# Performance work log

Measured on AMD Instinct MI355X. Metric: run time of the kernel, lower is better.

## Reference

```python
import jax, jax.numpy as jnp
import numpy as np
import math

H = 8
D_MODEL = 4096
D_K = D_MODEL // H  # 512; Sk must equal D_K for the im_attn @ value matmul
B, SQ, SK = 4, 2048, 512


def _linear_params(key, fan_in, fan_out):
    kw, kb = jax.random.split(key)
    bound = 1.0 / math.sqrt(fan_in)
    W = jax.random.uniform(kw, (fan_out, fan_in), jnp.float32, -bound, bound)
    b = jax.random.uniform(kb, (fan_out,), jnp.float32, -bound, bound)
    return W, b


def setup_inputs() -> dict:
    key = jax.random.key(0)
    ks = jax.random.split(key, 8)
    query = jax.random.normal(ks[0], (B, SQ, D_MODEL), jnp.float32)
    k_in = jax.random.normal(ks[1], (B, SK, D_MODEL), jnp.float32)
    v_in = jax.random.normal(ks[2], (B, SK, D_MODEL), jnp.float32)
    image_feat = jax.random.normal(ks[3], (B, SK, D_MODEL), jnp.float32)
    W0, b0 = _linear_params(ks[4], D_MODEL, D_MODEL)
    W1, b1 = _linear_params(ks[5], D_MODEL, D_MODEL)
    W2, b2 = _linear_params(ks[6], D_MODEL, D_MODEL)
    W3, b3 = _linear_params(ks[7], D_MODEL, D_MODEL)  # reused for image_feat AND output proj (as in source)
    return {"query": query, "key": k_in, "value": v_in, "image_feat": image_feat,
            "W0": W0, "b0": b0, "W1": W1, "b1": b1, "W2": W2, "b2": b2, "W3": W3, "b3": b3}


def _split_heads(x):
    # [b, s, d_model] -> [b, h, s, d_k]
    b, s, _ = x.shape
    return x.reshape(b, s, H, D_K).transpose(0, 2, 1, 3)


def reference(query, key, value, image_feat, W0, b0, W1, b1, W2, b2, W3, b3):
    q = _split_heads(query @ W0.T + b0)        # [b,h,Sq,d_k]
    k = _split_heads(key @ W1.T + b1)          # [b,h,Sk,d_k]
    v = _split_heads(value @ W2.T + b2)        # [b,h,Sk,d_k]
    imf = _split_heads(image_feat @ W3.T + b3) # [b,h,Sk,d_k]

    scores = jnp.einsum('bhqd,bhkd->bhqk', q, k) / math.sqrt(D_K)  # [b,h,Sq,Sk]
    p_attn = jax.nn.softmax(scores, axis=-1)
    # second-stage attention over feature axis (Sk == d_k so shapes line up)
    im_attn = jax.nn.softmax(jnp.einsum('bhqk,bhkd->bhqd', p_attn, imf), axis=-1)  # [b,h,Sq,d_k]
    x = jnp.einsum('bhqs,bhsd->bhqd', im_attn, v)  # contracts d_k axis of im_attn with Sk axis of v

    x = x.transpose(0, 2, 1, 3).reshape(query.shape[0], -1, H * D_K)  # [b,Sq,d_model]
    return x @ W3.T + b3  # linears[-1] is the same (shared) 4th linear
```

## Files before the change

### kernel.cpp

```cpp
#include <hip/hip_runtime.h>
#include <hip/hip_bf16.h>
#include <stdint.h>

#define B_   4
#define H_   8
#define SQ_  2048
#define SK_  512
#define DM_  4096
#define DK_  512

typedef __bf16 bf16;
typedef __bf16 bf16x8 __attribute__((ext_vector_type(8)));
typedef float  fx4    __attribute__((ext_vector_type(4)));

typedef __attribute__((address_space(1))) void gv_t;
typedef __attribute__((address_space(3))) void lv_t;

__global__ void sniff_dtype(const uint32_t* __restrict__ q, int* __restrict__ flag)
{
    const int l = threadIdx.x;
    int cnt = 0;
    #pragma unroll
    for (int i = 0; i < 4; ++i) {
        const uint32_t u = q[l * 4 + i];
        const int e = (u >> 7) & 0xFF;
        cnt += (e >= 100 && e <= 135) ? 1 : 0;
    }
    #pragma unroll
    for (int s = 1; s < 64; s <<= 1) cnt += __shfl_xor(cnt, s);
    if (l == 0) *flag = (cnt < 150) ? 1 : 0;
}

__global__ __launch_bounds__(256) void cvt_to_bf16(
    const void* __restrict__ in, bf16* __restrict__ out, const int* __restrict__ flagp)
{
    const size_t i = ((size_t)blockIdx.x * 256 + threadIdx.x) * 8;
    if (*flagp) {
        const float4* p = (const float4*)((const float*)in + i);
        const float4 u0 = p[0], u1 = p[1];
        bf16x8 v;
        v[0] = (bf16)u0.x; v[1] = (bf16)u0.y; v[2] = (bf16)u0.z; v[3] = (bf16)u0.w;
        v[4] = (bf16)u1.x; v[5] = (bf16)u1.y; v[6] = (bf16)u1.z; v[7] = (bf16)u1.w;
        *(bf16x8*)(out + i) = v;
    } else {
        *(bf16x8*)(out + i) = *(const bf16x8*)((const bf16*)in + i);
    }
}

__global__ __launch_bounds__(256, 3) void gemm_bt(
    const bf16* __restrict__ A, const bf16* __restrict__ Bt,
    void* __restrict__ Cv, const void* __restrict__ biasv,
    int K, int lda, int ldb, int ldc, float alpha,
    long long sAb, long long sAh, long long sBb, long long sBh,
    long long sCb, long long sCh,
    const int* __restrict__ flagp, int ebits)
{
    __shared__ bf16 sA[128 * 64];
    __shared__ bf16 sB[128 * 64];

    const int fl = ebits ? *flagp : 0;
    const bool bias32 = fl && (ebits & 1);
    const bool c32    = fl && (ebits & 2);

    const int z = blockIdx.z;
    const int bz = z >> 3, hz = z & 7;
    const bf16* Ab = A  + (size_t)bz * sAb + (size_t)hz * sAh;
    const bf16* Bb = Bt + (size_t)bz * sBb + (size_t)hz * sBh;
    const size_t offC = (size_t)bz * sCb + (size_t)hz * sCh;

    const int n0 = blockIdx.x * 128;
    const int m0 = blockIdx.y * 128;

    const int t = threadIdx.x;
    const int w = t >> 6, l = t & 63;
    const int lrow = l >> 3, lcol = l & 7;
    const int wm = (w >> 1) * 64, wn = (w & 1) * 64;
    const int ml = l & 15, quad = l >> 4;

    const bf16* pa[4];
    const bf16* pb[4];
    #pragma unroll
    for (int i = 0; i < 4; ++i) {
        const int c = w * 4 + i;
        const int r = c * 8 + lrow;
        const int jj = lcol ^ (r & 7);
        pa[i] = Ab + (size_t)(m0 + r) * lda + jj * 8;
        pb[i] = Bb + (size_t)(n0 + r) * ldb + jj * 8;
    }

    fx4 acc[4][4];
    const fx4 zero = {0.f, 0.f, 0.f, 0.f};
    #pragma unroll
    for (int i = 0; i < 4; ++i)
        #pragma unroll
        for (int j = 0; j < 4; ++j) acc[i][j] = zero;

    for (int kt = 0; kt < K; kt += 64) {
        #pragma unroll
        for (int i = 0; i < 4; ++i) {
            const int c = w * 4 + i;
            __builtin_amdgcn_global_load_lds((gv_t*)(pa[i] + kt), (lv_t*)(sA + c * 512), 16, 0, 0);
            __builtin_amdgcn_global_load_lds((gv_t*)(pb[i] + kt), (lv_t*)(sB + c * 512), 16, 0, 0);
        }
        __syncthreads();

        #pragma unroll
        for (int kk = 0; kk < 64; kk += 32) {
            bf16x8 af[4], bfr[4];
            const int jbase = (kk >> 3) + quad;
            #pragma unroll
            for (int mi = 0; mi < 4; ++mi) {
                const int r = wm + mi * 16 + ml;
                af[mi] = *(const bf16x8*)&sA[r * 64 + ((jbase ^ (r & 7)) << 3)];
            }
            #pragma unroll
            for (int ni = 0; ni < 4; ++ni) {
                const int r = wn + ni * 16 + ml;
                bfr[ni] = *(const bf16x8*)&sB[r * 64 + ((jbase ^ (r & 7)) << 3)];
            }
            #pragma unroll
            for (int mi = 0; mi < 4; ++mi)
                #pragma unroll
                for (int ni = 0; ni < 4; ++ni)
                    acc[mi][ni] = __builtin_amdgcn_mfma_f32_16x16x32_bf16(
                        af[mi], bfr[ni], acc[mi][ni], 0, 0, 0);
        }
        __syncthreads();
    }

    #pragma unroll
    for (int ni = 0; ni < 4; ++ni) {
        const int cg = n0 + wn + ni * 16 + ml;
        const float bv = biasv ? (bias32 ? ((const float*)biasv)[cg] : (float)((const bf16*)biasv)[cg]) : 0.f;
        #pragma unroll
        for (int mi = 0; mi < 4; ++mi) {
            const int rg = m0 + wm + mi * 16 + quad * 4;
            #pragma unroll
            for (int r = 0; r < 4; ++r) {
                const float val = acc[mi][ni][r] * alpha + bv;
                const size_t idx = offC + (size_t)(rg + r) * ldc + cg;
                if (c32) ((float*)Cv)[idx] = val;
                else     ((bf16*)Cv)[idx] = (bf16)val;
            }
        }
    }
}

__global__ __launch_bounds__(256) void softmax512(bf16* __restrict__ buf)
{
    const int row = blockIdx.x * 4 + (threadIdx.x >> 6);
    const int l = threadIdx.x & 63;
    bf16* p = buf + (size_t)row * 512 + l * 8;
    bf16x8 v = *(const bf16x8*)p;
    float f[8];
    float mx = -1e30f;
    #pragma unroll
    for (int j = 0; j < 8; ++j) {
        f[j] = (float)v[j];
        if (!(fabsf(f[j]) < 1e30f)) f[j] = -1e9f;
        mx = fmaxf(mx, f[j]);
    }
    #pragma unroll
    for (int s = 1; s < 64; s <<= 1) mx = fmaxf(mx, __shfl_xor(mx, s));
    float sum = 0.f;
    #pragma unroll
    for (int j = 0; j < 8; ++j) { f[j] = __expf(f[j] - mx); sum += f[j]; }
    #pragma unroll
    for (int s = 1; s < 64; s <<= 1) sum += __shfl_xor(sum, s);
    const float inv = 1.f / sum;
    #pragma unroll
    for (int j = 0; j < 8; ++j) v[j] = (bf16)(f[j] * inv);
    *(bf16x8*)p = v;
}

__global__ __launch_bounds__(256) void transpose_heads(
    const bf16* __restrict__ in, bf16* __restrict__ out)
{
    __shared__ bf16 tile[32][33];
    const int z = blockIdx.z, b = z >> 3, h = z & 7;
    const int s0 = blockIdx.x * 32, d0 = blockIdx.y * 32;
    const int tx = threadIdx.x, ty = threadIdx.y;
    #pragma unroll
    for (int j = 0; j < 4; ++j) {
        const int s = s0 + ty + j * 8;
        tile[ty + j * 8][tx] = in[(size_t)b * SK_ * DM_ + (size_t)s * DM_ + h * DK_ + d0 + tx];
    }
    __syncthreads();
    #pragma unroll
    for (int j = 0; j < 4; ++j) {
        const int d = d0 + ty + j * 8;
        out[(size_t)z * DK_ * SK_ + (size_t)d * SK_ + s0 + tx] = tile[tx][ty + j * 8];
    }
}

extern "C" void kernel_launch(void* const* d_in, const int* in_sizes, int n_in,
                              void* d_out, int out_size, void* d_ws, size_t ws_size,
                              hipStream_t stream)
{
    const void* query = d_in[0];
    const void* key   = d_in[1];
    const void* value = d_in[2];
    const void* imf   = d_in[3];
    const void* W0 = d_in[4];  const void* b0 = d_in[5];
    const void* W1 = d_in[6];  const void* b1 = d_in[7];
    const void* W2 = d_in[8];  const void* b2 = d_in[9];
    const void* W3 = d_in[10]; const void* b3 = d_in[11];

    bf16* ws    = (bf16*)d_ws;
    int*  flagp = (int*)d_ws;
    bf16* wslot = ws + 8;
    bf16* R     = ws + 8 + 16777216;
    bf16* inbuf = R;
    bf16* vproj = R + 8388608;
    bf16* imfp  = R + 16777216;
    bf16* s1    = R;
    bf16* xcat  = R;

    bf16* obase = (bf16*)d_out;
    bf16* qproj = obase;
    bf16* qbf   = obase + 33554432;
    bf16* kproj = obase + 33554432;
    bf16* vT    = obase + 41943040;
    bf16* imfT  = obase + 50331648;
    bf16* s2    = obase;

    const float inv_sqrt_dk = 0.04419417382415922f;

    sniff_dtype<<<1, 64, 0, stream>>>((const uint32_t*)query, flagp);

    cvt_to_bf16<<<16384, 256, 0, stream>>>(query, qbf, flagp);
    cvt_to_bf16<<<8192, 256, 0, stream>>>(W0, wslot, flagp);
    gemm_bt<<<dim3(32, 64, 1), 256, 0, stream>>>(qbf, wslot, qproj, b0,
        4096, 4096, 4096, 4096, 1.f, 0,0,0,0,0,0, flagp, 1);
    cvt_to_bf16<<<4096, 256, 0, stream>>>(key, inbuf, flagp);
    cvt_to_bf16<<<8192, 256, 0, stream>>>(W1, wslot, flagp);
    gemm_bt<<<dim3(32, 16, 1), 256, 0, stream>>>(inbuf, wslot, kproj, b1,
        4096, 4096, 4096, 4096, 1.f, 0,0,0,0,0,0, flagp, 1);
    cvt_to_bf16<<<4096, 256, 0, stream>>>(value, inbuf, flagp);
    cvt_to_bf16<<<8192, 256, 0, stream>>>(W2, wslot, flagp);
    gemm_bt<<<dim3(32, 16, 1), 256, 0, stream>>>(inbuf, wslot, vproj, b2,
        4096, 4096, 4096, 4096, 1.f, 0,0,0,0,0,0, flagp, 1);
    cvt_to_bf16<<<4096, 256, 0, stream>>>(imf, inbuf, flagp);
    cvt_to_bf16<<<8192, 256, 0, stream>>>(W3, wslot, flagp);
    gemm_bt<<<dim3(32, 16, 1), 256, 0, stream>>>(inbuf, wslot, imfp, b3,
        4096, 4096, 4096, 4096, 1.f, 0,0,0,0,0,0, flagp, 1);

    transpose_heads<<<dim3(16, 16, 32), dim3(32, 8), 0, stream>>>(vproj, vT);
    transpose_heads<<<dim3(16, 16, 32), dim3(32, 8), 0, stream>>>(imfp, imfT);

    gemm_bt<<<dim3(4, 16, 32), 256, 0, stream>>>(qproj, kproj, s1, nullptr,
        512, 4096, 4096, 512, inv_sqrt_dk,
        (long long)SQ_*DM_, (long long)DK_, (long long)SK_*DM_, (long long)DK_,
        (long long)H_*SQ_*SK_, (long long)SQ_*SK_, flagp, 0);
    softmax512<<<dim3(16384), 256, 0, stream>>>(s1);
    gemm_bt<<<dim3(4, 16, 32), 256, 0, stream>>>(s1, imfT, s2, nullptr,
        512, 512, 512, 512, 1.f,
        (long long)H_*SQ_*SK_, (long long)SQ_*SK_, (long long)H_*DK_*SK_, (long long)DK_*SK_,
        (long long)H_*SQ_*SK_, (long long)SQ_*SK_, flagp, 0);
    softmax512<<<dim3(16384), 256, 0, stream>>>(s2);
    gemm_bt<<<dim3(4, 16, 32), 256, 0, stream>>>(s2, vT, xcat, nullptr,
        512, 512, 512, 4096, 1.f,
        (long long)H_*SQ_*SK_, (long long)SQ_*SK_, (long long)H_*DK_*SK_, (long long)DK_*SK_,
        (long long)SQ_*DM_, (long long)DK_, flagp, 0);
    cvt_to_bf16<<<8192, 256, 0, stream>>>(W3, wslot, flagp);
    gemm_bt<<<dim3(32, 64, 1), 256, 0, stream>>>(xcat, wslot, d_out, b3,
        4096, 4096, 4096, 4096, 1.f, 0,0,0,0,0,0, flagp, 3);
}
```

Before: 1.685 ms.

## Add 256x256-tile double-buffered GEMM and use it for large projections and attention

Adds a new 512-thread GEMM kernel with 256x256 output tiles. It double-buffers K-tiles in LDS through direct global-to-LDS loads, uses an XOR swizzle, raises wave priority around the MFMA blocks, and remaps workgroup indices across XCDs. The kernel replaces the 128-tile gemm_bt for the query and output projections and for the three batched attention GEMMs, to raise arithmetic intensity and overlap loads with compute. The larger tiles use 128 KB of LDS and many accumulator registers, which limits occupancy. The grid for the attention GEMMs also shrinks to 512 workgroups.

```diff
diff --git a/kernel.cpp b/kernel.cpp
--- a/kernel.cpp
+++ b/kernel.cpp
@@ -146,6 +146,150 @@
     }
 }
 
+#define ISSUE_TILE(tt, bb)                                                        \
+    do {                                                                          \
+        _Pragma("unroll")                                                         \
+        for (int i_ = 0; i_ < 4; ++i_) {                                          \
+            const int c_ = w * 4 + i_;                                            \
+            __builtin_amdgcn_global_load_lds((gv_t*)(pa[i_] + (size_t)(tt) * 64), \
+                (lv_t*)(&sm[bb][0][c_ * 512]), 16, 0, 0);                         \
+            __builtin_amdgcn_global_load_lds((gv_t*)(pb[i_] + (size_t)(tt) * 64), \
+                (lv_t*)(&sm[bb][1][c_ * 512]), 16, 0, 0);                         \
+        }                                                                         \
+    } while (0)
+
+__global__ __launch_bounds__(512, 2) void gemm256(
+    const bf16* __restrict__ A, const bf16* __restrict__ Bt,
+    void* __restrict__ Cv, const void* __restrict__ biasv,
+    int K, int lda, int ldb, int ldc, float alpha,
+    long long sAb, long long sAh, long long sBb, long long sBh,
+    long long sCb, long long sCh,
+    const int* __restrict__ flagp, int ebits)
+{
+    __shared__ bf16 sm[2][2][256 * 64];
+
+    const int fl = ebits ? *flagp : 0;
+    const bool bias32 = fl && (ebits & 1);
+    const bool c32    = fl && (ebits & 2);
+
+    const int gX = gridDim.x, gY = gridDim.y;
+    int idx = (blockIdx.z * gY + blockIdx.y) * gX + blockIdx.x;
+    const int nwg = gX * gY * gridDim.z;
+    if ((nwg & 7) == 0) idx = (idx & 7) * (nwg >> 3) + (idx >> 3);
+    const int bx = idx % gX;
+    const int tmpi = idx / gX;
+    const int by = tmpi % gY;
+    const int z  = tmpi / gY;
+
+    const int bz = z >> 3, hz = z & 7;
+    const bf16* Ab = A  + (size_t)bz * sAb + (size_t)hz * sAh;
+    const bf16* Bb = Bt + (size_t)bz * sBb + (size_t)hz * sBh;
+    const size_t offC = (size_t)bz * sCb + (size_t)hz * sCh;
+
+    const int n0 = bx * 256;
+    const int m0 = by * 256;
+
+    const int t  = threadIdx.x;
+    const int w  = t >> 6, l = t & 63;
+    const int lrow = l >> 3, lcol = l & 7;
+    const int wr = w >> 2, wc = w & 3;
+    const int R0 = wr * 128, C0 = wc * 64;
+    const int ml = l & 15, quad = l >> 4;
+
+    const bf16* pa[4];
+    const bf16* pb[4];
+    #pragma unroll
+    for (int i = 0; i < 4; ++i) {
+        const int c = w * 4 + i;
+        const int r = c * 8 + lrow;
+        const int jj = lcol ^ (r & 7);
+        pa[i] = Ab + (size_t)(m0 + r) * lda + jj * 8;
+        pb[i] = Bb + (size_t)(n0 + r) * ldb + jj * 8;
+    }
+
+    fx4 acc[8][4];
+    const fx4 zero = {0.f, 0.f, 0.f, 0.f};
+    #pragma unroll
+    for (int i = 0; i < 8; ++i)
+        #pragma unroll
+        for (int j = 0; j < 4; ++j) acc[i][j] = zero;
+
+    const int nt = K >> 6;
+
+    ISSUE_TILE(0, 0);
+    ISSUE_TILE(1, 1);
+    asm volatile("s_waitcnt vmcnt(8)" ::: "memory");
+    asm volatile("s_barrier" ::: "memory");
+
+    for (int tt = 0; tt < nt; ++tt) {
+        const int b = tt & 1;
+        const bf16* sA = sm[b][0];
+        const bf16* sB = sm[b][1];
+
+        #pragma unroll
+        for (int q = 0; q < 4; ++q) {
+            const int mh = q >> 1, nh = q & 1;
+            bf16x8 af[4][2], bfr[2][2];
+            #pragma unroll
+            for (int im = 0; im < 4; ++im)
+                #pragma unroll
+                for (int kI = 0; kI < 2; ++kI) {
+                    const int fr = R0 + (mh * 4 + im) * 16 + ml;
+                    const int j  = kI * 4 + quad;
+                    af[im][kI] = *(const bf16x8*)&sA[fr * 64 + ((j ^ (fr & 7)) << 3)];
+                }
+            #pragma unroll
+            for (int in = 0; in < 2; ++in)
+                #pragma unroll
+                for (int kI = 0; kI < 2; ++kI) {
+                    const int fr = C0 + (nh * 2 + in) * 16 + ml;
+                    const int j  = kI * 4 + quad;
+                    bfr[in][kI] = *(const bf16x8*)&sB[fr * 64 + ((j ^ (fr & 7)) << 3)];
+                }
+            asm volatile("s_barrier" ::: "memory");
+            __builtin_amdgcn_s_setprio(1);
+            #pragma unroll
+            for (int kI = 0; kI < 2; ++kI)
+                #pragma unroll
+                for (int im = 0; im < 4; ++im)
+                    #pragma unroll
+                    for (int in = 0; in < 2; ++in)
+                        acc[mh * 4 + im][nh * 2 + in] =
+                            __builtin_amdgcn_mfma_f32_16x16x32_bf16(
+                                af[im][kI], bfr[in][kI],
+                                acc[mh * 4 + im][nh * 2 + in], 0, 0, 0);
+            __builtin_amdgcn_s_setprio(0);
+            asm volatile("s_barrier" ::: "memory");
+        }
+
+        if (tt + 1 >= nt) break;
+        if (tt + 2 < nt) {
+            ISSUE_TILE(tt + 2, b);
+            asm volatile("s_waitcnt vmcnt(8)" ::: "memory");
+        } else {
+            asm volatile("s_waitcnt vmcnt(0)" ::: "memory");
+        }
+        asm volatile("s_barrier" ::: "memory");
+    }
+
+    #pragma unroll
+    for (int ni = 0; ni < 4; ++ni) {
+        const int cg = n0 + C0 + ni * 16 + ml;
+        const float bv = biasv ? (bias32 ? ((const float*)biasv)[cg] : (float)((const bf16*)biasv)[cg]) : 0.f;
+        #pragma unroll
+        for (int mi = 0; mi < 8; ++mi) {
+            const int rg = m0 + R0 + mi * 16 + quad * 4;
+            #pragma unroll
+            for (int r = 0; r < 4; ++r) {
+                const float val = acc[mi][ni][r] * alpha + bv;
+                const size_t idx = offC + (size_t)(rg + r) * ldc + cg;
+                if (c32) ((float*)Cv)[idx] = val;
+                else     ((bf16*)Cv)[idx] = (bf16)val;
+            }
+        }
+    }
+}
+
 __global__ __launch_bounds__(256) void softmax512(bf16* __restrict__ buf)
 {
     const int row = blockIdx.x * 4 + (threadIdx.x >> 6);
@@ -230,7 +374,7 @@
 
     cvt_to_bf16<<<16384, 256, 0, stream>>>(query, qbf, flagp);
     cvt_to_bf16<<<8192, 256, 0, stream>>>(W0, wslot, flagp);
-    gemm_bt<<<dim3(32, 64, 1), 256, 0, stream>>>(qbf, wslot, qproj, b0,
+    gemm256<<<dim3(16, 32, 1), 512, 0, stream>>>(qbf, wslot, qproj, b0,
         4096, 4096, 4096, 4096, 1.f, 0,0,0,0,0,0, flagp, 1);
     cvt_to_bf16<<<4096, 256, 0, stream>>>(key, inbuf, flagp);
     cvt_to_bf16<<<8192, 256, 0, stream>>>(W1, wslot, flagp);
@@ -248,21 +392,21 @@
     transpose_heads<<<dim3(16, 16, 32), dim3(32, 8), 0, stream>>>(vproj, vT);
     transpose_heads<<<dim3(16, 16, 32), dim3(32, 8), 0, stream>>>(imfp, imfT);
 
-    gemm_bt<<<dim3(4, 16, 32), 256, 0, stream>>>(qproj, kproj, s1, nullptr,
+    gemm256<<<dim3(2, 8, 32), 512, 0, stream>>>(qproj, kproj, s1, nullptr,
         512, 4096, 4096, 512, inv_sqrt_dk,
         (long long)SQ_*DM_, (long long)DK_, (long long)SK_*DM_, (long long)DK_,
         (long long)H_*SQ_*SK_, (long long)SQ_*SK_, flagp, 0);
     softmax512<<<dim3(16384), 256, 0, stream>>>(s1);
-    gemm_bt<<<dim3(4, 16, 32), 256, 0, stream>>>(s1, imfT, s2, nullptr,
+    gemm256<<<dim3(2, 8, 32), 512, 0, stream>>>(s1, imfT, s2, nullptr,
         512, 512, 512, 512, 1.f,
         (long long)H_*SQ_*SK_, (long long)SQ_*SK_, (long long)H_*DK_*SK_, (long long)DK_*SK_,
         (long long)H_*SQ_*SK_, (long long)SQ_*SK_, flagp, 0);
     softmax512<<<dim3(16384), 256, 0, stream>>>(s2);
-    gemm_bt<<<dim3(4, 16, 32), 256, 0, stream>>>(s2, vT, xcat, nullptr,
+    gemm256<<<dim3(2, 8, 32), 512, 0, stream>>>(s2, vT, xcat, nullptr,
         512, 512, 512, 4096, 1.f,
         (long long)H_*SQ_*SK_, (long long)SQ_*SK_, (long long)H_*DK_*SK_, (long long)DK_*SK_,
         (long long)SQ_*DM_, (long long)DK_, flagp, 0);
     cvt_to_bf16<<<8192, 256, 0, stream>>>(W3, wslot, flagp);
-    gemm_bt<<<dim3(32, 64, 1), 256, 0, stream>>>(xcat, wslot, d_out, b3,
+    gemm256<<<dim3(16, 32, 1), 512, 0, stream>>>(xcat, wslot, d_out, b3,
         4096, 4096, 4096, 4096, 1.f, 0,0,0,0,0,0, flagp, 3);
 }
```

Measured after the change: 1.750 ms. 3.9% more time.
